# Performance work log

Hardware: AMD Instinct MI355X
Metric: run time of the kernel (lower is better)

Reference implementation:

```python
import jax, jax.numpy as jnp
import numpy as np

M, IN, H, OUT = 64, 3, 256, 3
B = 8192
W0_FIRST = 30.0
W0_HIDDEN = 30.0


def setup_inputs() -> dict:
    key = jax.random.key(0)
    ks = jax.random.split(key, 12)
    fb = 1.0 / IN                                   # first-layer bound
    hb = np.sqrt(6.0 / H) / W0_HIDDEN               # hidden bound
    x = jax.random.uniform(ks[0], (B, IN), jnp.float32, -1.0, 1.0)
    w0 = jax.random.uniform(ks[1], (M, H, IN), jnp.float32, -fb, fb)
    b0 = jnp.zeros((M, H), jnp.float32)
    w1 = jax.random.uniform(ks[2], (M, H, H), jnp.float32, -hb, hb)
    b1 = jnp.zeros((M, H), jnp.float32)
    w2 = jax.random.uniform(ks[3], (M, H, H), jnp.float32, -hb, hb)
    b2 = jnp.zeros((M, H), jnp.float32)
    w3 = jax.random.uniform(ks[4], (M, H, H), jnp.float32, -hb, hb)
    b3 = jnp.zeros((M, H), jnp.float32)
    wf = jax.random.uniform(ks[5], (M, OUT, H), jnp.float32, -hb, hb)
    bf = jnp.zeros((M, OUT), jnp.float32)
    return {"x": x, "w0": w0, "b0": b0, "w1": w1, "b1": b1,
            "w2": w2, "b2": b2, "w3": w3, "b3": b3, "wf": wf, "bf": bf}


def reference(x, w0, b0, w1, b1, w2, b2, w3, b3, wf, bf):
    # first sine layer: [B,in] x [M,H,in] -> [B,M,H]
    h = jnp.sin(W0_FIRST * (jnp.einsum('bi,moi->bmo', x, w0) + b0[None]))
    # hidden sine layers
    for w, b in ((w1, b1), (w2, b2), (w3, b3)):
        h = jnp.sin(W0_HIDDEN * (jnp.einsum('bmi,moi->bmo', h, w) + b[None]))
    # final linear: [B,M,H] x [M,out,H] -> [B,M,out]
    return jnp.einsum('bmi,moi->bmo', h, wf) + bf[None]
```

## Files before the change

kernel.cpp:

```cpp
#include <hip/hip_runtime.h>

#define MEXP  64
#define HDIM  256
#define INDIM 3
#define ODIM  3
#define BT    128
#define NTILE 64
#define SINSC 4.774648292756860f

typedef __attribute__((ext_vector_type(8))) _Float16 f16x8;
typedef __attribute__((ext_vector_type(4))) _Float16 f16x4;
typedef __attribute__((ext_vector_type(4))) float    f32x4;

__device__ __forceinline__ int swz(int row, int byteInRow) {
  return (row * 512 + byteInRow) ^ (((row ^ (row >> 3)) & 7) << 4);
}

__global__ void prep_hidden(const float* __restrict__ w1, const float* __restrict__ w2,
                            const float* __restrict__ w3, _Float16* __restrict__ ws) {
  int chunk = blockIdx.x * 256 + threadIdx.x;
  int lm    = chunk >> 13;
  int c     = chunk & 8191;
  int layer = lm >> 6, m = lm & 63;
  int lane  = c & 63;
  int ctks  = c >> 6;
  int ct = ctks >> 3, ks = ctks & 7;
  int col = ct * 16 + (lane & 15);
  int k   = ks * 32 + ((lane >> 4) << 3);
  const float* w = (layer == 0) ? w1 : (layer == 1) ? w2 : w3;
  const float* src = w + ((size_t)m * HDIM + col) * HDIM + k;
  f16x8 v;
#pragma unroll
  for (int j = 0; j < 8; ++j) v[j] = (_Float16)(src[j] * SINSC);
  *(f16x8*)(ws + (size_t)chunk * 8) = v;
}

__global__ void prep_wf(const float* __restrict__ wf, _Float16* __restrict__ ws) {
  int chunk = blockIdx.x * 256 + threadIdx.x;
  int m    = chunk >> 9;
  int c    = chunk & 511;
  int lane = c & 63;
  int ks   = c >> 6;
  int col  = lane & 15;
  int k    = ks * 32 + ((lane >> 4) << 3);
  f16x8 v;
  if (col < ODIM) {
    const float* src = wf + ((size_t)m * ODIM + col) * HDIM + k;
#pragma unroll
    for (int j = 0; j < 8; ++j) v[j] = (_Float16)src[j];
  } else {
#pragma unroll
    for (int j = 0; j < 8; ++j) v[j] = (_Float16)0.0f;
  }
  *(f16x8*)(ws + (size_t)chunk * 8) = v;
}

__device__ __forceinline__ void hidden_layer(char* hb, const _Float16* __restrict__ wl,
                                             const float* __restrict__ bptr,
                                             int wid, int lane, int g) {
  f32x4 acc[8][2] = {};
  const f16x8* wfrag = (const f16x8*)wl;
  int ct0 = wid * 2, ct1 = ct0 + 1;
  f16x8 A0 = wfrag[(ct0 * 8 + 0) * 64 + lane];
  f16x8 A1 = wfrag[(ct1 * 8 + 0) * 64 + lane];
#pragma unroll
  for (int ks = 0; ks < 8; ++ks) {
    f16x8 a0 = A0, a1 = A1;
    if (ks < 7) {
      A0 = wfrag[(ct0 * 8 + ks + 1) * 64 + lane];
      A1 = wfrag[(ct1 * 8 + ks + 1) * 64 + lane];
    }
#pragma unroll
    for (int rt = 0; rt < 8; ++rt) {
      f16x8 b = *(const f16x8*)(hb + swz(rt * 16 + (lane & 15), ks * 64 + g * 16));
      acc[rt][0] = __builtin_amdgcn_mfma_f32_16x16x32_f16(a0, b, acc[rt][0], 0, 0, 0);
      acc[rt][1] = __builtin_amdgcn_mfma_f32_16x16x32_f16(a1, b, acc[rt][1], 0, 0, 0);
    }
  }
  __syncthreads();
#pragma unroll
  for (int ct = 0; ct < 2; ++ct) {
    int c0 = wid * 32 + ct * 16 + g * 4;
    f32x4 bias = *(const f32x4*)(bptr + c0);
#pragma unroll
    for (int rt = 0; rt < 8; ++rt) {
      f16x4 v;
#pragma unroll
      for (int t = 0; t < 4; ++t)
        v[t] = (_Float16)__builtin_amdgcn_sinf(fmaf(bias[t], SINSC, acc[rt][ct][t]));
      *(f16x4*)(hb + swz(rt * 16 + (lane & 15), c0 * 2)) = v;
    }
  }
  __syncthreads();
}

__global__ __launch_bounds__(512, 2)
void siren_fused(const float* __restrict__ x, const float* __restrict__ w0,
                 const float* __restrict__ b0, const float* __restrict__ b1,
                 const float* __restrict__ b2, const float* __restrict__ b3,
                 const float* __restrict__ bfin, const _Float16* __restrict__ wh,
                 const _Float16* __restrict__ wff, float* __restrict__ out) {
  __shared__ _Float16 hbuf[BT * HDIM];
  char* hb = (char*)hbuf;

  int tid  = threadIdx.x;
  int lane = tid & 63;
  int wid  = tid >> 6;
  int g    = lane >> 4;
  int id   = blockIdx.x;
  int m    = ((id & 7) << 3) + ((id >> 3) >> 6);
  int tile = (id >> 3) & (NTILE - 1);

  {
    int col  = tid & 255;
    int half = tid >> 8;
    const float* wp = w0 + ((size_t)m * HDIM + col) * INDIM;
    float wc0 = wp[0], wc1 = wp[1], wc2 = wp[2];
    float bc  = b0[m * HDIM + col] * SINSC;
    const float* xp = x + ((size_t)tile * BT + half * 64) * INDIM;
#pragma unroll 4
    for (int r = 0; r < 64; ++r) {
      float z = fmaf(xp[r * 3 + 2], wc2, fmaf(xp[r * 3 + 1], wc1, xp[r * 3] * wc0));
      float h = __builtin_amdgcn_sinf(fmaf(z, SINSC, bc));
      *(_Float16*)(hb + swz(half * 64 + r, col * 2)) = (_Float16)h;
    }
  }
  __syncthreads();

  hidden_layer(hb, wh + ((size_t)0 * MEXP + m) * (HDIM * HDIM), b1 + m * HDIM, wid, lane, g);
  hidden_layer(hb, wh + ((size_t)1 * MEXP + m) * (HDIM * HDIM), b2 + m * HDIM, wid, lane, g);
  hidden_layer(hb, wh + ((size_t)2 * MEXP + m) * (HDIM * HDIM), b3 + m * HDIM, wid, lane, g);

  {
    f32x4 facc = {};
    const f16x8* wfrag = (const f16x8*)(wff + (size_t)m * (16 * HDIM));
#pragma unroll
    for (int ks = 0; ks < 8; ++ks) {
      f16x8 b = *(const f16x8*)(hb + swz(wid * 16 + (lane & 15), ks * 64 + g * 16));
      f16x8 a = wfrag[ks * 64 + lane];
      facc = __builtin_amdgcn_mfma_f32_16x16x32_f16(a, b, facc, 0, 0, 0);
    }
    if (g == 0) {
      size_t r = (size_t)tile * BT + wid * 16 + (lane & 15);
#pragma unroll
      for (int t = 0; t < 3; ++t)
        out[(r * MEXP + m) * ODIM + t] = facc[t] + bfin[m * ODIM + t];
    }
  }
}

extern "C" void kernel_launch(void* const* d_in, const int* in_sizes, int n_in,
                              void* d_out, int out_size, void* d_ws, size_t ws_size,
                              hipStream_t stream) {
  (void)in_sizes; (void)n_in; (void)out_size; (void)ws_size;
  const float* x  = (const float*)d_in[0];
  const float* w0 = (const float*)d_in[1];
  const float* b0 = (const float*)d_in[2];
  const float* w1 = (const float*)d_in[3];
  const float* b1 = (const float*)d_in[4];
  const float* w2 = (const float*)d_in[5];
  const float* b2 = (const float*)d_in[6];
  const float* w3 = (const float*)d_in[7];
  const float* b3 = (const float*)d_in[8];
  const float* wf = (const float*)d_in[9];
  const float* bf = (const float*)d_in[10];

  _Float16* wh  = (_Float16*)d_ws;
  _Float16* wff = wh + (size_t)3 * MEXP * HDIM * HDIM;

  prep_hidden<<<6144, 256, 0, stream>>>(w1, w2, w3, wh);
  prep_wf<<<128, 256, 0, stream>>>(wf, wff);
  siren_fused<<<4096, 512, 0, stream>>>(x, w0, b0, b1, b2, b3, bf, wh, wff, (float*)d_out);
}
```

Before: 387.1 us.

## Halve batch tile, widen per-wave column tiles, fold bias into accumulator init

Measured after the change: 531.0 us. 1.37x slower.

```diff
diff --git a/kernel.cpp b/kernel.cpp
--- a/kernel.cpp
+++ b/kernel.cpp
@@ -4,8 +4,8 @@
 #define HDIM  256
 #define INDIM 3
 #define ODIM  3
-#define BT    128
-#define NTILE 64
+#define BT    64
+#define NTILE 128
 #define SINSC 4.774648292756860f
 
 typedef __attribute__((ext_vector_type(8))) _Float16 f16x8;
@@ -58,43 +58,54 @@
 __device__ __forceinline__ void hidden_layer(char* hb, const _Float16* __restrict__ wl,
                                              const float* __restrict__ bptr,
                                              int wid, int lane, int g) {
-  f32x4 acc[8][2] = {};
+  f32x4 acc[4][4];
+#pragma unroll
+  for (int ct = 0; ct < 4; ++ct) {
+    f32x4 binit = *(const f32x4*)(bptr + wid * 64 + ct * 16 + g * 4);
+    binit *= SINSC;
+#pragma unroll
+    for (int rt = 0; rt < 4; ++rt) acc[rt][ct] = binit;
+  }
   const f16x8* wfrag = (const f16x8*)wl;
-  int ct0 = wid * 2, ct1 = ct0 + 1;
-  f16x8 A0 = wfrag[(ct0 * 8 + 0) * 64 + lane];
-  f16x8 A1 = wfrag[(ct1 * 8 + 0) * 64 + lane];
+  f16x8 A[4];
+#pragma unroll
+  for (int ct = 0; ct < 4; ++ct)
+    A[ct] = wfrag[((wid * 4 + ct) * 8 + 0) * 64 + lane];
 #pragma unroll
   for (int ks = 0; ks < 8; ++ks) {
-    f16x8 a0 = A0, a1 = A1;
+    f16x8 a[4];
+#pragma unroll
+    for (int ct = 0; ct < 4; ++ct) a[ct] = A[ct];
     if (ks < 7) {
-      A0 = wfrag[(ct0 * 8 + ks + 1) * 64 + lane];
-      A1 = wfrag[(ct1 * 8 + ks + 1) * 64 + lane];
+#pragma unroll
+      for (int ct = 0; ct < 4; ++ct)
+        A[ct] = wfrag[((wid * 4 + ct) * 8 + ks + 1) * 64 + lane];
     }
 #pragma unroll
-    for (int rt = 0; rt < 8; ++rt) {
+    for (int rt = 0; rt < 4; ++rt) {
       f16x8 b = *(const f16x8*)(hb + swz(rt * 16 + (lane & 15), ks * 64 + g * 16));
-      acc[rt][0] = __builtin_amdgcn_mfma_f32_16x16x32_f16(a0, b, acc[rt][0], 0, 0, 0);
-      acc[rt][1] = __builtin_amdgcn_mfma_f32_16x16x32_f16(a1, b, acc[rt][1], 0, 0, 0);
+#pragma unroll
+      for (int ct = 0; ct < 4; ++ct)
+        acc[rt][ct] = __builtin_amdgcn_mfma_f32_16x16x32_f16(a[ct], b, acc[rt][ct], 0, 0, 0);
     }
   }
   __syncthreads();
 #pragma unroll
-  for (int ct = 0; ct < 2; ++ct) {
-    int c0 = wid * 32 + ct * 16 + g * 4;
-    f32x4 bias = *(const f32x4*)(bptr + c0);
+  for (int ct = 0; ct < 4; ++ct) {
+    int c0 = wid * 64 + ct * 16 + g * 4;
 #pragma unroll
-    for (int rt = 0; rt < 8; ++rt) {
+    for (int rt = 0; rt < 4; ++rt) {
       f16x4 v;
 #pragma unroll
       for (int t = 0; t < 4; ++t)
-        v[t] = (_Float16)__builtin_amdgcn_sinf(fmaf(bias[t], SINSC, acc[rt][ct][t]));
+        v[t] = (_Float16)__builtin_amdgcn_sinf(acc[rt][ct][t]);
       *(f16x4*)(hb + swz(rt * 16 + (lane & 15), c0 * 2)) = v;
     }
   }
   __syncthreads();
 }
 
-__global__ __launch_bounds__(512, 2)
+__global__ __launch_bounds__(256, 4)
 void siren_fused(const float* __restrict__ x, const float* __restrict__ w0,
                  const float* __restrict__ b0, const float* __restrict__ b1,
                  const float* __restrict__ b2, const float* __restrict__ b3,
@@ -108,21 +119,20 @@
   int wid  = tid >> 6;
   int g    = lane >> 4;
   int id   = blockIdx.x;
-  int m    = ((id & 7) << 3) + ((id >> 3) >> 6);
+  int m    = ((id & 7) << 3) + ((id >> 3) >> 7);
   int tile = (id >> 3) & (NTILE - 1);
 
   {
-    int col  = tid & 255;
-    int half = tid >> 8;
+    int col = tid;
     const float* wp = w0 + ((size_t)m * HDIM + col) * INDIM;
     float wc0 = wp[0], wc1 = wp[1], wc2 = wp[2];
     float bc  = b0[m * HDIM + col] * SINSC;
-    const float* xp = x + ((size_t)tile * BT + half * 64) * INDIM;
+    const float* xp = x + (size_t)tile * BT * INDIM;
 #pragma unroll 4
-    for (int r = 0; r < 64; ++r) {
+    for (int r = 0; r < BT; ++r) {
       float z = fmaf(xp[r * 3 + 2], wc2, fmaf(xp[r * 3 + 1], wc1, xp[r * 3] * wc0));
       float h = __builtin_amdgcn_sinf(fmaf(z, SINSC, bc));
-      *(_Float16*)(hb + swz(half * 64 + r, col * 2)) = (_Float16)h;
+      *(_Float16*)(hb + swz(r, col * 2)) = (_Float16)h;
     }
   }
   __syncthreads();
@@ -170,5 +180,5 @@
 
   prep_hidden<<<6144, 256, 0, stream>>>(w1, w2, w3, wh);
   prep_wf<<<128, 256, 0, stream>>>(wf, wff);
-  siren_fused<<<4096, 512, 0, stream>>>(x, w0, b0, b1, b2, b3, bf, wh, wff, (float*)d_out);
+  siren_fused<<<8192, 256, 0, stream>>>(x, w0, b0, b1, b2, b3, bf, wh, wff, (float*)d_out);
 }
```
